# Optimization experiments

Measured on AMD Instinct MI355X. Metric: run time of the kernel, lower is better.

The kernel has to match this reference:

```python
import jax, jax.numpy as jnp
import numpy as np

BUFFER_C = 1.25

def setup_inputs() -> dict:
    key = jax.random.key(0)
    k1, k2, k3 = jax.random.split(key, 3)
    T, D, E = 4096, 1024, 8
    x = jax.random.normal(k1, (T, D), dtype=jnp.float32)
    Wg = jax.random.normal(k2, (D, E), dtype=jnp.float32) / np.sqrt(D)
    bg = jnp.zeros((E,), dtype=jnp.float32)
    W = jax.random.normal(k3, (E, D, D), dtype=jnp.float32) / np.sqrt(D)
    b = jnp.zeros((E, D), dtype=jnp.float32)
    return {"x": x, "Wg": Wg, "bg": bg, "W": W, "b": b}


def reference(x, Wg, bg, W, b):
    # Top-1 (Switch-style) routing with capacity buffer, per-expert Linear,
    # prob-weighted combine, plus load-balancing aux loss.
    T, D = x.shape
    E = W.shape[0]
    capacity = int(BUFFER_C * T / E)

    logits = x @ Wg + bg                      # [T, E]
    probs = jax.nn.softmax(logits, axis=-1)   # [T, E]
    top_idx = jnp.argmax(probs, axis=-1)      # [T]
    top_prob = jnp.take_along_axis(probs, top_idx[:, None], axis=-1)[:, 0]

    onehot = jax.nn.one_hot(top_idx, E, dtype=x.dtype)       # [T, E]
    # 1-indexed position of each token within its expert's buffer
    pos = jnp.cumsum(onehot, axis=0) * onehot                # [T, E]
    dispatch = jnp.where((onehot > 0) & (pos <= capacity), 1.0, 0.0).astype(x.dtype)

    # dense dispatch/combine equivalent of the masked per-expert loop
    xe = jnp.einsum('te,td->etd', dispatch, x)               # [E, T, D]
    ye = jnp.einsum('etd,edf->etf', xe, W) + b[:, None, :]   # [E, T, D]
    y = jnp.einsum('te,etf->tf', dispatch, ye)               # [T, D] (0 for dropped)
    out = y * top_prob[:, None]

    # aux load-balance loss: E * sum_e f_e * P_e
    f = onehot.mean(axis=0)
    P = probs.mean(axis=0)
    aux_loss = E * jnp.sum(f * P)
    return out, aux_loss
```

## Files before the change

kernel.cpp:

```cpp
#include <hip/hip_runtime.h>
#include <hip/hip_bf16.h>
#include <cstdint>

#define T_TOK 4096
#define D_DIM 1024
#define E_EXP 8
#define CAP   640
#define NBIN  64
#define MAXDROP 3456

typedef __attribute__((ext_vector_type(8))) short short8;
typedef __attribute__((ext_vector_type(4))) float f32x4;

__device__ inline unsigned short f2bf(float f) {
    uint32_t u = __float_as_uint(f);
    u += 0x7fffu + ((u >> 16) & 1u);
    return (unsigned short)(u >> 16);
}

__global__ __launch_bounds__(256) void gating_kernel(
    const float* __restrict__ x, const float* __restrict__ Wg,
    const float* __restrict__ bg,
    int* __restrict__ top_idx, float* __restrict__ top_prob,
    float* __restrict__ ppart)
{
    int wid  = threadIdx.x >> 6;
    int lane = threadIdx.x & 63;
    int t = blockIdx.x * 4 + wid;

    float acc[8];
    #pragma unroll
    for (int e = 0; e < 8; e++) acc[e] = 0.f;

    const float* xr = x + (size_t)t * D_DIM;
    #pragma unroll 4
    for (int i = 0; i < 16; i++) {
        int d = lane + 64 * i;
        float xv = xr[d];
        const float4* wr = (const float4*)(Wg + (size_t)d * 8);
        float4 w0 = wr[0], w1 = wr[1];
        acc[0] += xv * w0.x; acc[1] += xv * w0.y;
        acc[2] += xv * w0.z; acc[3] += xv * w0.w;
        acc[4] += xv * w1.x; acc[5] += xv * w1.y;
        acc[6] += xv * w1.z; acc[7] += xv * w1.w;
    }
    #pragma unroll
    for (int off = 32; off > 0; off >>= 1) {
        #pragma unroll
        for (int e = 0; e < 8; e++) acc[e] += __shfl_xor(acc[e], off, 64);
    }

    if (lane == 0) {
        float lg[8];
        #pragma unroll
        for (int e = 0; e < 8; e++) lg[e] = acc[e] + bg[e];
        float m = lg[0]; int am = 0;
        #pragma unroll
        for (int e = 1; e < 8; e++) { if (lg[e] > m) { m = lg[e]; am = e; } }
        float ex[8], s = 0.f;
        #pragma unroll
        for (int e = 0; e < 8; e++) { ex[e] = expf(lg[e] - m); s += ex[e]; }
        float inv = 1.f / s;
        top_idx[t]  = am;
        top_prob[t] = ex[am] * inv;
        int bin = (int)(blockIdx.x & (NBIN - 1));
        #pragma unroll
        for (int e = 0; e < 8; e++) atomicAdd(&ppart[bin * 8 + e], ex[e] * inv);
    }
}

__global__ __launch_bounds__(1024) void scan_kernel(
    const int* __restrict__ top_idx,
    int* __restrict__ tok_list, int* __restrict__ cnt, int* __restrict__ fullcnt,
    float* __restrict__ out)
{
    __shared__ int counts[64][8];
    __shared__ int excl[64][8];
    __shared__ int droplist[MAXDROP];
    __shared__ int ndrop;

    int tid  = threadIdx.x;
    int wv   = tid >> 6;
    int lane = tid & 63;
    unsigned long long ltmask = (lane == 0) ? 0ull : ((~0ull) >> (64 - lane));

    if (tid == 0) ndrop = 0;

    int ecache[4];
    #pragma unroll
    for (int c = 0; c < 4; c++)
        ecache[c] = top_idx[(4 * wv + c) * 64 + lane];

    #pragma unroll
    for (int c = 0; c < 4; c++) {
        int chunk = 4 * wv + c;
        int e = ecache[c];
        #pragma unroll
        for (int q = 0; q < 8; q++) {
            unsigned long long mk = __ballot(e == q);
            int tot = __popcll(mk);
            if (lane == q) counts[chunk][q] = tot;
        }
    }
    __syncthreads();

    if (wv == 0) {
        #pragma unroll
        for (int q = 0; q < 8; q++) {
            int v = counts[lane][q];
            int orig = v;
            #pragma unroll
            for (int off = 1; off < 64; off <<= 1) {
                int n = __shfl_up(v, off, 64);
                if (lane >= off) v += n;
            }
            excl[lane][q] = v - orig;
            int total = __shfl(v, 63, 64);
            if (lane == 0) {
                fullcnt[q] = total;
                cnt[q] = total < CAP ? total : CAP;
            }
        }
    }
    __syncthreads();

    #pragma unroll
    for (int c = 0; c < 4; c++) {
        int chunk = 4 * wv + c;
        int t = chunk * 64 + lane;
        int e = ecache[c];
        int pos = 0;
        #pragma unroll
        for (int q = 0; q < 8; q++) {
            unsigned long long mk = __ballot(e == q);
            if (e == q) pos = excl[chunk][q] + __popcll(mk & ltmask);
        }
        if (pos < CAP) {
            tok_list[e * CAP + pos] = t;
        } else {
            int di = atomicAdd(&ndrop, 1);
            droplist[di] = t;
        }
    }
    __syncthreads();

    int nd = ndrop;
    int grp = tid >> 8;
    int col = (tid & 255) * 4;
    float4 z = {0.f, 0.f, 0.f, 0.f};
    for (int d = grp; d < nd; d += 4) {
        int row = droplist[d];
        *(float4*)&out[(size_t)row * D_DIM + col] = z;
    }
}

__device__ inline void stage_tile(const float* __restrict__ x,
                                  const float* __restrict__ We, int n0,
                                  const int* rowtok, int k0,
                                  int a_c4, int a_r0, int b_c4, int b_kk,
                                  short* Als, short* Bls)
{
    #pragma unroll
    for (int i = 0; i < 4; i++) {
        const float4 xv = *(const float4*)(x + (size_t)rowtok[i] * D_DIM + k0 + 4 * a_c4);
        ushort4 us;
        us.x = f2bf(xv.x); us.y = f2bf(xv.y); us.z = f2bf(xv.z); us.w = f2bf(xv.w);
        *(ushort4*)&Als[(a_r0 + 32 * i) * 40 + 4 * a_c4] = us;
    }
    const float* wp = We + (size_t)(k0 + b_kk) * D_DIM + n0 + 4 * b_c4;
    float4 w0 = *(const float4*)(wp);
    float4 w1 = *(const float4*)(wp + D_DIM);
    ushort2 u;
    u.x = f2bf(w0.x); u.y = f2bf(w1.x);
    *(ushort2*)&Bls[(4 * b_c4 + 0) * 40 + b_kk] = u;
    u.x = f2bf(w0.y); u.y = f2bf(w1.y);
    *(ushort2*)&Bls[(4 * b_c4 + 1) * 40 + b_kk] = u;
    u.x = f2bf(w0.z); u.y = f2bf(w1.z);
    *(ushort2*)&Bls[(4 * b_c4 + 2) * 40 + b_kk] = u;
    u.x = f2bf(w0.w); u.y = f2bf(w1.w);
    *(ushort2*)&Bls[(4 * b_c4 + 3) * 40 + b_kk] = u;
}

__global__ __launch_bounds__(256) void expert_gemm(
    const float* __restrict__ x, const float* __restrict__ W,
    const float* __restrict__ bias,
    const int* __restrict__ tok_list, const int* __restrict__ cnt,
    const float* __restrict__ top_prob, float* __restrict__ out)
{
    int bid = blockIdx.x;
    int e   = bid / 80;
    int rem = bid % 80;
    int mt  = rem / 16, nt = rem % 16;
    int count = cnt[e];
    int m0 = mt * 128;
    if (m0 >= count) return;
    int n0 = nt * 64;

    __shared__ __attribute__((aligned(16))) short AlsBuf[2][128 * 40];
    __shared__ __attribute__((aligned(16))) short BlsBuf[2][64 * 40];

    int tid  = threadIdx.x;
    int lane = tid & 63, wid = tid >> 6;
    int quad = lane >> 4, l16 = lane & 15;
    int mB = (wid >> 1) * 64, nB = (wid & 1) * 32;

    f32x4 accf[4][2];
    #pragma unroll
    for (int i = 0; i < 4; i++)
        #pragma unroll
        for (int j = 0; j < 2; j++)
            accf[i][j] = (f32x4){0.f, 0.f, 0.f, 0.f};

    const int* tl = tok_list + e * CAP;
    int a_c4 = tid & 7,  a_r0 = tid >> 3;
    int b_c4 = tid & 15, b_kk = (tid >> 4) * 2;
    const float* We = W + (size_t)e * D_DIM * D_DIM;

    int rowtok[4];
    #pragma unroll
    for (int i = 0; i < 4; i++) {
        int gm = m0 + a_r0 + 32 * i;
        rowtok[i] = tl[gm < count ? gm : 0];
    }

    stage_tile(x, We, n0, rowtok, 0, a_c4, a_r0, b_c4, b_kk, AlsBuf[0], BlsBuf[0]);
    __syncthreads();

    int cur = 0;
    for (int k0 = 0; k0 < D_DIM; k0 += 32) {
        int nxt = cur ^ 1;
        if (k0 + 32 < D_DIM)
            stage_tile(x, We, n0, rowtok, k0 + 32, a_c4, a_r0, b_c4, b_kk,
                       AlsBuf[nxt], BlsBuf[nxt]);

        const short* Als = AlsBuf[cur];
        const short* Bls = BlsBuf[cur];
        short8 af[4], bfr[2];
        #pragma unroll
        for (int i = 0; i < 4; i++)
            af[i] = *(const short8*)&Als[(mB + 16 * i + l16) * 40 + quad * 8];
        #pragma unroll
        for (int j = 0; j < 2; j++)
            bfr[j] = *(const short8*)&Bls[(nB + 16 * j + l16) * 40 + quad * 8];
        #pragma unroll
        for (int i = 0; i < 4; i++)
            #pragma unroll
            for (int j = 0; j < 2; j++)
                accf[i][j] = __builtin_amdgcn_mfma_f32_16x16x32_bf16(af[i], bfr[j], accf[i][j], 0, 0, 0);

        __syncthreads();
        cur = nxt;
    }

    float bv[2];
    #pragma unroll
    for (int j = 0; j < 2; j++)
        bv[j] = bias[e * D_DIM + n0 + nB + 16 * j + l16];

    #pragma unroll
    for (int i = 0; i < 4; i++) {
        int rb = m0 + mB + 16 * i + quad * 4;
        #pragma unroll
        for (int r = 0; r < 4; r++) {
            int gm = rb + r;
            if (gm >= count) continue;
            int tok = tl[gm];
            float p = top_prob[tok];
            float* orow = out + (size_t)tok * D_DIM + n0 + nB + l16;
            #pragma unroll
            for (int j = 0; j < 2; j++)
                orow[16 * j] = (accf[i][j][r] + bv[j]) * p;
        }
    }
}

__global__ void aux_kernel(const float* __restrict__ ppart, const int* __restrict__ fullcnt,
                           float* __restrict__ out_aux) {
    int lane = threadIdx.x;
    float p[8];
    #pragma unroll
    for (int e = 0; e < 8; e++) p[e] = ppart[lane * 8 + e];
    #pragma unroll
    for (int off = 32; off > 0; off >>= 1) {
        #pragma unroll
        for (int e = 0; e < 8; e++) p[e] += __shfl_xor(p[e], off, 64);
    }
    if (lane == 0) {
        float s = 0.f;
        #pragma unroll
        for (int e = 0; e < 8; e++)
            s += ((float)fullcnt[e] / (float)T_TOK) * (p[e] / (float)T_TOK);
        out_aux[0] = (float)E_EXP * s;
    }
}

extern "C" void kernel_launch(void* const* d_in, const int* in_sizes, int n_in,
                              void* d_out, int out_size, void* d_ws, size_t ws_size,
                              hipStream_t stream) {
    const float* x  = (const float*)d_in[0];
    const float* Wg = (const float*)d_in[1];
    const float* bg = (const float*)d_in[2];
    const float* W  = (const float*)d_in[3];
    const float* b  = (const float*)d_in[4];
    float* out = (float*)d_out;

    char* ws = (char*)d_ws;
    int*   top_idx  = (int*)(ws + 0);
    float* top_prob = (float*)(ws + 16384);
    int*   tok_list = (int*)(ws + 32768);
    int*   cnt      = (int*)(ws + 53248);
    int*   fullcnt  = (int*)(ws + 53280);
    float* ppart    = (float*)(ws + 53312);

    hipMemsetAsync(ppart, 0, NBIN * 8 * sizeof(float), stream);
    hipLaunchKernelGGL(gating_kernel, dim3(T_TOK / 4), dim3(256), 0, stream,
                       x, Wg, bg, top_idx, top_prob, ppart);
    hipLaunchKernelGGL(scan_kernel, dim3(1), dim3(1024), 0, stream,
                       top_idx, tok_list, cnt, fullcnt, out);
    hipLaunchKernelGGL(expert_gemm, dim3(E_EXP * 5 * 16), dim3(256), 0, stream,
                       x, W, b, tok_list, cnt, top_prob, out);
    hipLaunchKernelGGL(aux_kernel, dim3(1), dim3(64), 0, stream, ppart, fullcnt,
                       out + (size_t)T_TOK * D_DIM);
}
```

Before: 171.9 us.

## Pre-convert x and W to bf16, stream GEMM tiles via global_load_lds

```diff
diff --git a/kernel.cpp b/kernel.cpp
--- a/kernel.cpp
+++ b/kernel.cpp
@@ -8,6 +8,7 @@
 #define CAP   640
 #define NBIN  64
 #define MAXDROP 3456
+#define MT    10
 
 typedef __attribute__((ext_vector_type(8))) short short8;
 typedef __attribute__((ext_vector_type(4))) float f32x4;
@@ -18,54 +19,97 @@
     return (unsigned short)(u >> 16);
 }
 
-__global__ __launch_bounds__(256) void gating_kernel(
+__device__ inline void dma16(const void* g, void* l) {
+    __builtin_amdgcn_global_load_lds(
+        (const __attribute__((address_space(1))) unsigned int*)g,
+        (__attribute__((address_space(3))) unsigned int*)l, 16, 0, 0);
+}
+
+__global__ __launch_bounds__(256) void prep_kernel(
     const float* __restrict__ x, const float* __restrict__ Wg,
-    const float* __restrict__ bg,
-    int* __restrict__ top_idx, float* __restrict__ top_prob,
-    float* __restrict__ ppart)
+    const float* __restrict__ bg, const float* __restrict__ W,
+    unsigned short* __restrict__ xb, unsigned short* __restrict__ Wb,
+    int* __restrict__ top_idx, float* __restrict__ top_prob, float* __restrict__ ppart)
 {
-    int wid  = threadIdx.x >> 6;
-    int lane = threadIdx.x & 63;
-    int t = blockIdx.x * 4 + wid;
-
-    float acc[8];
-    #pragma unroll
-    for (int e = 0; e < 8; e++) acc[e] = 0.f;
-
-    const float* xr = x + (size_t)t * D_DIM;
-    #pragma unroll 4
-    for (int i = 0; i < 16; i++) {
-        int d = lane + 64 * i;
-        float xv = xr[d];
-        const float4* wr = (const float4*)(Wg + (size_t)d * 8);
-        float4 w0 = wr[0], w1 = wr[1];
-        acc[0] += xv * w0.x; acc[1] += xv * w0.y;
-        acc[2] += xv * w0.z; acc[3] += xv * w0.w;
-        acc[4] += xv * w1.x; acc[5] += xv * w1.y;
-        acc[6] += xv * w1.z; acc[7] += xv * w1.w;
-    }
-    #pragma unroll
-    for (int off = 32; off > 0; off >>= 1) {
-        #pragma unroll
-        for (int e = 0; e < 8; e++) acc[e] += __shfl_xor(acc[e], off, 64);
-    }
-
-    if (lane == 0) {
-        float lg[8];
-        #pragma unroll
-        for (int e = 0; e < 8; e++) lg[e] = acc[e] + bg[e];
-        float m = lg[0]; int am = 0;
-        #pragma unroll
-        for (int e = 1; e < 8; e++) { if (lg[e] > m) { m = lg[e]; am = e; } }
-        float ex[8], s = 0.f;
-        #pragma unroll
-        for (int e = 0; e < 8; e++) { ex[e] = expf(lg[e] - m); s += ex[e]; }
-        float inv = 1.f / s;
-        top_idx[t]  = am;
-        top_prob[t] = ex[am] * inv;
-        int bin = (int)(blockIdx.x & (NBIN - 1));
-        #pragma unroll
-        for (int e = 0; e < 8; e++) atomicAdd(&ppart[bin * 8 + e], ex[e] * inv);
+    int bid = blockIdx.x;
+    int tid = threadIdx.x;
+
+    if (bid < 2048) {
+        __shared__ unsigned short tile[64][68];
+        int e  = bid >> 8;
+        int k0 = ((bid >> 4) & 15) * 64;
+        int n0 = (bid & 15) * 64;
+        const float* Wsrc = W + (size_t)e * D_DIM * D_DIM;
+        #pragma unroll
+        for (int p = 0; p < 4; p++) {
+            int kk = p * 16 + (tid >> 4);
+            int nn = (tid & 15) * 4;
+            float4 v = *(const float4*)(Wsrc + (size_t)(k0 + kk) * D_DIM + n0 + nn);
+            ushort4 u;
+            u.x = f2bf(v.x); u.y = f2bf(v.y); u.z = f2bf(v.z); u.w = f2bf(v.w);
+            *(ushort4*)&tile[kk][nn] = u;
+        }
+        __syncthreads();
+        unsigned short* Wdst = Wb + (size_t)e * D_DIM * D_DIM;
+        #pragma unroll
+        for (int p = 0; p < 2; p++) {
+            int n = p * 32 + (tid >> 3);
+            int g = tid & 7;
+            short8 v;
+            #pragma unroll
+            for (int z = 0; z < 8; z++) v[z] = (short)tile[g * 8 + z][n];
+            *(short8*)&Wdst[(size_t)(n0 + n) * D_DIM + k0 + g * 8] = v;
+        }
+    } else {
+        int wid  = tid >> 6;
+        int lane = tid & 63;
+        int t = (bid - 2048) * 4 + wid;
+
+        float acc[8];
+        #pragma unroll
+        for (int e = 0; e < 8; e++) acc[e] = 0.f;
+
+        const float* xr = x + (size_t)t * D_DIM;
+        #pragma unroll
+        for (int i = 0; i < 4; i++) {
+            int d0 = i * 256 + lane * 4;
+            float4 xv = *(const float4*)(xr + d0);
+            ushort4 u;
+            u.x = f2bf(xv.x); u.y = f2bf(xv.y); u.z = f2bf(xv.z); u.w = f2bf(xv.w);
+            *(ushort4*)&xb[(size_t)t * D_DIM + d0] = u;
+            float xs[4] = {xv.x, xv.y, xv.z, xv.w};
+            #pragma unroll
+            for (int j = 0; j < 4; j++) {
+                const float4* wr = (const float4*)(Wg + (size_t)(d0 + j) * 8);
+                float4 w0 = wr[0], w1 = wr[1];
+                acc[0] += xs[j] * w0.x; acc[1] += xs[j] * w0.y;
+                acc[2] += xs[j] * w0.z; acc[3] += xs[j] * w0.w;
+                acc[4] += xs[j] * w1.x; acc[5] += xs[j] * w1.y;
+                acc[6] += xs[j] * w1.z; acc[7] += xs[j] * w1.w;
+            }
+        }
+        #pragma unroll
+        for (int off = 32; off > 0; off >>= 1) {
+            #pragma unroll
+            for (int e = 0; e < 8; e++) acc[e] += __shfl_xor(acc[e], off, 64);
+        }
+        if (lane == 0) {
+            float lg[8];
+            #pragma unroll
+            for (int e = 0; e < 8; e++) lg[e] = acc[e] + bg[e];
+            float m = lg[0]; int am = 0;
+            #pragma unroll
+            for (int e = 1; e < 8; e++) { if (lg[e] > m) { m = lg[e]; am = e; } }
+            float ex[8], s = 0.f;
+            #pragma unroll
+            for (int e = 0; e < 8; e++) { ex[e] = expf(lg[e] - m); s += ex[e]; }
+            float inv = 1.f / s;
+            top_idx[t]  = am;
+            top_prob[t] = ex[am] * inv;
+            int bin = (int)(bid & (NBIN - 1));
+            #pragma unroll
+            for (int e = 0; e < 8; e++) atomicAdd(&ppart[bin * 8 + e], ex[e] * inv);
+        }
     }
 }
 
@@ -154,122 +198,99 @@
     }
 }
 
-__device__ inline void stage_tile(const float* __restrict__ x,
-                                  const float* __restrict__ We, int n0,
-                                  const int* rowtok, int k0,
-                                  int a_c4, int a_r0, int b_c4, int b_kk,
-                                  short* Als, short* Bls)
+__device__ inline void stage_dma(const unsigned short* gA, const unsigned short* gB,
+                                 unsigned short (*Ab)[64][8], unsigned short (*Bb)[64][8],
+                                 int k0, int w)
 {
-    #pragma unroll
-    for (int i = 0; i < 4; i++) {
-        const float4 xv = *(const float4*)(x + (size_t)rowtok[i] * D_DIM + k0 + 4 * a_c4);
-        ushort4 us;
-        us.x = f2bf(xv.x); us.y = f2bf(xv.y); us.z = f2bf(xv.z); us.w = f2bf(xv.w);
-        *(ushort4*)&Als[(a_r0 + 32 * i) * 40 + 4 * a_c4] = us;
-    }
-    const float* wp = We + (size_t)(k0 + b_kk) * D_DIM + n0 + 4 * b_c4;
-    float4 w0 = *(const float4*)(wp);
-    float4 w1 = *(const float4*)(wp + D_DIM);
-    ushort2 u;
-    u.x = f2bf(w0.x); u.y = f2bf(w1.x);
-    *(ushort2*)&Bls[(4 * b_c4 + 0) * 40 + b_kk] = u;
-    u.x = f2bf(w0.y); u.y = f2bf(w1.y);
-    *(ushort2*)&Bls[(4 * b_c4 + 1) * 40 + b_kk] = u;
-    u.x = f2bf(w0.z); u.y = f2bf(w1.z);
-    *(ushort2*)&Bls[(4 * b_c4 + 2) * 40 + b_kk] = u;
-    u.x = f2bf(w0.w); u.y = f2bf(w1.w);
-    *(ushort2*)&Bls[(4 * b_c4 + 3) * 40 + b_kk] = u;
+    dma16(gA + k0 + w * 8,       &Ab[w][0][0]);
+    dma16(gA + k0 + (w + 4) * 8, &Ab[w + 4][0][0]);
+    dma16(gB + k0 + w * 8,       &Bb[w][0][0]);
+    dma16(gB + k0 + (w + 4) * 8, &Bb[w + 4][0][0]);
 }
 
 __global__ __launch_bounds__(256) void expert_gemm(
-    const float* __restrict__ x, const float* __restrict__ W,
+    const unsigned short* __restrict__ xb, const unsigned short* __restrict__ Wb,
     const float* __restrict__ bias,
     const int* __restrict__ tok_list, const int* __restrict__ cnt,
     const float* __restrict__ top_prob, float* __restrict__ out)
 {
     int bid = blockIdx.x;
-    int e   = bid / 80;
-    int rem = bid % 80;
-    int mt  = rem / 16, nt = rem % 16;
+    int e   = bid / (MT * 16);
+    int rem = bid % (MT * 16);
+    int mt  = rem >> 4, nt = rem & 15;
     int count = cnt[e];
-    int m0 = mt * 128;
+    int m0 = mt * 64;
     if (m0 >= count) return;
     int n0 = nt * 64;
 
-    __shared__ __attribute__((aligned(16))) short AlsBuf[2][128 * 40];
-    __shared__ __attribute__((aligned(16))) short BlsBuf[2][64 * 40];
+    __shared__ unsigned short Ab[2][8][64][8];
+    __shared__ unsigned short Bb[2][8][64][8];
 
     int tid  = threadIdx.x;
-    int lane = tid & 63, wid = tid >> 6;
+    int lane = tid & 63, w = tid >> 6;
     int quad = lane >> 4, l16 = lane & 15;
-    int mB = (wid >> 1) * 64, nB = (wid & 1) * 32;
-
-    f32x4 accf[4][2];
-    #pragma unroll
-    for (int i = 0; i < 4; i++)
+    int mw = (w >> 1) * 32, nw = (w & 1) * 32;
+
+    const int* tl = tok_list + e * CAP;
+    int ra = m0 + lane; if (ra >= count) ra = count - 1;
+    int tokA = tl[ra];
+    const unsigned short* gA = xb + (size_t)tokA * D_DIM;
+    const unsigned short* gB = Wb + (size_t)e * D_DIM * D_DIM + (size_t)(n0 + lane) * D_DIM;
+
+    f32x4 acc[2][2];
+    #pragma unroll
+    for (int i = 0; i < 2; i++)
         #pragma unroll
         for (int j = 0; j < 2; j++)
-            accf[i][j] = (f32x4){0.f, 0.f, 0.f, 0.f};
-
-    const int* tl = tok_list + e * CAP;
-    int a_c4 = tid & 7,  a_r0 = tid >> 3;
-    int b_c4 = tid & 15, b_kk = (tid >> 4) * 2;
-    const float* We = W + (size_t)e * D_DIM * D_DIM;
-
-    int rowtok[4];
-    #pragma unroll
-    for (int i = 0; i < 4; i++) {
-        int gm = m0 + a_r0 + 32 * i;
-        rowtok[i] = tl[gm < count ? gm : 0];
-    }
-
-    stage_tile(x, We, n0, rowtok, 0, a_c4, a_r0, b_c4, b_kk, AlsBuf[0], BlsBuf[0]);
-    __syncthreads();
+            acc[i][j] = (f32x4){0.f, 0.f, 0.f, 0.f};
+
+    stage_dma(gA, gB, Ab[0], Bb[0], 0, w);
 
     int cur = 0;
-    for (int k0 = 0; k0 < D_DIM; k0 += 32) {
-        int nxt = cur ^ 1;
-        if (k0 + 32 < D_DIM)
-            stage_tile(x, We, n0, rowtok, k0 + 32, a_c4, a_r0, b_c4, b_kk,
-                       AlsBuf[nxt], BlsBuf[nxt]);
-
-        const short* Als = AlsBuf[cur];
-        const short* Bls = BlsBuf[cur];
-        short8 af[4], bfr[2];
-        #pragma unroll
-        for (int i = 0; i < 4; i++)
-            af[i] = *(const short8*)&Als[(mB + 16 * i + l16) * 40 + quad * 8];
-        #pragma unroll
-        for (int j = 0; j < 2; j++)
-            bfr[j] = *(const short8*)&Bls[(nB + 16 * j + l16) * 40 + quad * 8];
-        #pragma unroll
-        for (int i = 0; i < 4; i++)
-            #pragma unroll
-            for (int j = 0; j < 2; j++)
-                accf[i][j] = __builtin_amdgcn_mfma_f32_16x16x32_bf16(af[i], bfr[j], accf[i][j], 0, 0, 0);
-
+    #pragma unroll 1
+    for (int kt = 0; kt < 16; kt++) {
         __syncthreads();
-        cur = nxt;
+        if (kt + 1 < 16)
+            stage_dma(gA, gB, Ab[cur ^ 1], Bb[cur ^ 1], (kt + 1) * 64, w);
+
+        short8 af[2][2], bf[2][2];
+        #pragma unroll
+        for (int s = 0; s < 2; s++) {
+            #pragma unroll
+            for (int i = 0; i < 2; i++) {
+                af[s][i] = *(const short8*)&Ab[cur][s * 4 + quad][mw + 16 * i + l16][0];
+                bf[s][i] = *(const short8*)&Bb[cur][s * 4 + quad][nw + 16 * i + l16][0];
+            }
+        }
+        #pragma unroll
+        for (int s = 0; s < 2; s++)
+            #pragma unroll
+            for (int i = 0; i < 2; i++)
+                #pragma unroll
+                for (int j = 0; j < 2; j++)
+                    acc[i][j] = __builtin_amdgcn_mfma_f32_16x16x32_bf16(
+                        af[s][i], bf[s][j], acc[i][j], 0, 0, 0);
+        cur ^= 1;
     }
 
     float bv[2];
     #pragma unroll
     for (int j = 0; j < 2; j++)
-        bv[j] = bias[e * D_DIM + n0 + nB + 16 * j + l16];
-
-    #pragma unroll
-    for (int i = 0; i < 4; i++) {
-        int rb = m0 + mB + 16 * i + quad * 4;
+        bv[j] = bias[e * D_DIM + n0 + nw + 16 * j + l16];
+
+    #pragma unroll
+    for (int i = 0; i < 2; i++) {
+        int rb = m0 + mw + 16 * i + quad * 4;
         #pragma unroll
         for (int r = 0; r < 4; r++) {
             int gm = rb + r;
             if (gm >= count) continue;
             int tok = tl[gm];
             float p = top_prob[tok];
-            float* orow = out + (size_t)tok * D_DIM + n0 + nB + l16;
+            float* orow = out + (size_t)tok * D_DIM + n0 + nw + l16;
             #pragma unroll
             for (int j = 0; j < 2; j++)
-                orow[16 * j] = (accf[i][j][r] + bv[j]) * p;
+                orow[16 * j] = (acc[i][j][r] + bv[j]) * p;
         }
     }
 }
@@ -305,20 +326,22 @@
     float* out = (float*)d_out;
 
     char* ws = (char*)d_ws;
-    int*   top_idx  = (int*)(ws + 0);
-    float* top_prob = (float*)(ws + 16384);
-    int*   tok_list = (int*)(ws + 32768);
-    int*   cnt      = (int*)(ws + 53248);
-    int*   fullcnt  = (int*)(ws + 53280);
-    float* ppart    = (float*)(ws + 53312);
+    unsigned short* xb = (unsigned short*)(ws + 0);
+    unsigned short* Wb = (unsigned short*)(ws + 8388608);
+    int*   top_idx  = (int*)(ws + 25165824);
+    float* top_prob = (float*)(ws + 25182208);
+    int*   tok_list = (int*)(ws + 25198592);
+    int*   cnt      = (int*)(ws + 25219072);
+    int*   fullcnt  = (int*)(ws + 25219104);
+    float* ppart    = (float*)(ws + 25219136);
 
     hipMemsetAsync(ppart, 0, NBIN * 8 * sizeof(float), stream);
-    hipLaunchKernelGGL(gating_kernel, dim3(T_TOK / 4), dim3(256), 0, stream,
-                       x, Wg, bg, top_idx, top_prob, ppart);
+    hipLaunchKernelGGL(prep_kernel, dim3(2048 + T_TOK / 4), dim3(256), 0, stream,
+                       x, Wg, bg, W, xb, Wb, top_idx, top_prob, ppart);
     hipLaunchKernelGGL(scan_kernel, dim3(1), dim3(1024), 0, stream,
                        top_idx, tok_list, cnt, fullcnt, out);
-    hipLaunchKernelGGL(expert_gemm, dim3(E_EXP * 5 * 16), dim3(256), 0, stream,
-                       x, W, b, tok_list, cnt, top_prob, out);
+    hipLaunchKernelGGL(expert_gemm, dim3(E_EXP * MT * 16), dim3(256), 0, stream,
+                       xb, Wb, b, tok_list, cnt, top_prob, out);
     hipLaunchKernelGGL(aux_kernel, dim3(1), dim3(64), 0, stream, ppart, fullcnt,
                        out + (size_t)T_TOK * D_DIM);
 }
```

Measured after the change: 191.1 us. 11.2% more time.
